# Optimization experiments

Hardware: AMD Instinct MI355X
Metric: run time of the kernel (lower is better)

## Reference

```python
import jax, jax.numpy as jnp
import numpy as np

L_MAX = 6          # L_in = L_out = (0, 6)
N = 2048           # batch / node count
C = 256            # channels (channel_wise => in == out)
NUM_ORDERS = (L_MAX + 1) ** 2  # 49


def _so2_indices(lmax):
    """Replicates equitorch _so2_indices for L_in = L_out = (0, lmax)."""
    entries = []
    widx = 0
    for l_out in range(lmax + 1):
        for l_in in range(lmax + 1):
            for m_w in range(-min(l_out, l_in), min(l_out, l_in) + 1):
                pairs = [(-abs(m_w), -m_w), (abs(m_w), m_w)] if m_w != 0 else [(0, 0)]
                for m_out, m_in in pairs:
                    i_out = l_out * l_out + l_out + m_out  # degree_order_to_index, l_min=0
                    i_in = l_in * l_in + l_in + m_in
                    sign = -1.0 if (m_out > 0 and m_in < 0) else 1.0
                    entries.append((i_out, i_in, l_in, l_out, sign, widx))
                widx += 1
    entries.sort()
    M_out = np.array([e[0] for e in entries], np.int32)
    M_in = np.array([e[1] for e in entries], np.int32)
    sign = np.array([e[4] for e in entries], np.float32)
    w_idx = np.array([e[5] for e in entries], np.int32)
    return M_out, M_in, sign, w_idx, widx


def setup_inputs() -> dict:
    key = jax.random.key(0)
    k1, k2 = jax.random.split(key)
    M_out, M_in, sign, w_idx, num_weights = _so2_indices(L_MAX)
    x = jax.random.normal(k1, (N, NUM_ORDERS, C), dtype=jnp.float32)
    weight = jax.random.normal(k2, (1, num_weights, C), dtype=jnp.float32)
    return {
        "x": x,
        "weight": weight,
        "weight_sign": jnp.asarray(sign),
        "M_in": jnp.asarray(M_in),
        "M_out": jnp.asarray(M_out),
        "weight_index": jnp.asarray(w_idx),
    }


def reference(x, weight, weight_sign, M_in, M_out, weight_index):
    # gather input orders: [N, P, C], P = 413 gathered (m_out, m_in) pairs
    X = x[:, M_in, :]
    # gather per-(l_out,l_in,m) channel-wise weights and apply sign: [1, P, C]
    W = weight[:, weight_index, :] * weight_sign[None, :, None]
    out = X * W  # channel-wise product
    # scatter-add into output orders: [N, num_orders_out, C]
    return jnp.zeros((x.shape[0], NUM_ORDERS, x.shape[2]), x.dtype).at[:, M_out, :].add(out)
```

## Files before the change

### kernel.cpp

```cpp
#include <hip/hip_runtime.h>


#define LMAX 6
#define NORD 49
#define NENT 413
#define C4   64
#define NW   8
#define BLK  512

struct Meta {
  unsigned packed[NENT];
  int gstart[NORD + 1];
  int wbeg[NW + 1];
};

constexpr Meta make_meta() {
  Meta m{};
  int io[NENT] = {}, ii[NENT] = {}, wi[NENT] = {}, sg[NENT] = {};
  int cnt = 0, widx = 0;
  for (int lo = 0; lo <= LMAX; ++lo) {
    for (int li = 0; li <= LMAX; ++li) {
      int mn = lo < li ? lo : li;
      for (int mw = -mn; mw <= mn; ++mw) {
        if (mw == 0) {
          io[cnt] = lo * lo + lo; ii[cnt] = li * li + li;
          wi[cnt] = widx; sg[cnt] = 0; ++cnt;
        } else {
          int a = mw > 0 ? mw : -mw;
          io[cnt] = lo * lo + lo - a; ii[cnt] = li * li + li - mw;
          wi[cnt] = widx; sg[cnt] = 0; ++cnt;
          io[cnt] = lo * lo + lo + a; ii[cnt] = li * li + li + mw;
          wi[cnt] = widx; sg[cnt] = (mw < 0) ? 1 : 0; ++cnt;
        }
        ++widx;
      }
    }
  }
  int slot[NORD * NORD];
  for (int k = 0; k < NORD * NORD; ++k) slot[k] = -1;
  for (int e = 0; e < cnt; ++e) slot[io[e] * NORD + ii[e]] = e;
  int order[NENT] = {};
  int s = 0;
  for (int k = 0; k < NORD * NORD; ++k)
    if (slot[k] >= 0) order[s++] = slot[k];
  int gc[NORD] = {};
  for (int e = 0; e < cnt; ++e) gc[io[e]]++;
  m.gstart[0] = 0;
  for (int g = 0; g < NORD; ++g) m.gstart[g + 1] = m.gstart[g] + gc[g];
  for (int t = 0; t < cnt; ++t) {
    int e = order[t];
    m.packed[t] = (unsigned)ii[e] | ((unsigned)wi[e] << 8) | ((unsigned)sg[e] << 31);
  }
  m.wbeg[0] = 0; m.wbeg[NW] = NORD;
  for (int y = 1; y < NW; ++y) {
    int target = (cnt * y) / NW;
    int g = m.wbeg[y - 1] + 1;
    while (g < NORD && m.gstart[g] < target) ++g;
    if (g - 1 > m.wbeg[y - 1] &&
        (m.gstart[g] - target) > (target - m.gstart[g - 1])) --g;
    int maxg = NORD - (NW - y);
    if (g > maxg) g = maxg;
    m.wbeg[y] = g;
  }
  return m;
}

static constexpr Meta g_meta = make_meta();

template <int E, int E1>
struct Ent {
  __device__ static inline void run(float4& acc, const float4* __restrict__ xs,
                                    const float4* __restrict__ wg, int lane) {
    constexpr unsigned p = g_meta.packed[E];
    constexpr int mi = (int)(p & 255u);
    constexpr int wix = (int)((p >> 8) & 0x3FFu);
    constexpr bool neg = (p & 0x80000000u) != 0u;
    float4 xv = xs[mi * C4 + lane];
    float4 wv = wg[wix * C4 + lane];
    if constexpr (neg) {
      acc.x = fmaf(-xv.x, wv.x, acc.x);
      acc.y = fmaf(-xv.y, wv.y, acc.y);
      acc.z = fmaf(-xv.z, wv.z, acc.z);
      acc.w = fmaf(-xv.w, wv.w, acc.w);
    } else {
      acc.x = fmaf(xv.x, wv.x, acc.x);
      acc.y = fmaf(xv.y, wv.y, acc.y);
      acc.z = fmaf(xv.z, wv.z, acc.z);
      acc.w = fmaf(xv.w, wv.w, acc.w);
    }
    Ent<E + 1, E1>::run(acc, xs, wg, lane);
  }
};
template <int E1>
struct Ent<E1, E1> {
  __device__ static inline void run(float4&, const float4*, const float4*, int) {}
};

template <int G, int G1>
struct Grp {
  __device__ static inline void run(const float4* __restrict__ xs,
                                    const float4* __restrict__ wg,
                                    float4* __restrict__ og, int lane) {
    float4 acc = make_float4(0.f, 0.f, 0.f, 0.f);
    Ent<g_meta.gstart[G], g_meta.gstart[G + 1]>::run(acc, xs, wg, lane);
    og[G * C4 + lane] = acc;
    Grp<G + 1, G1>::run(xs, wg, og, lane);
  }
};
template <int G1>
struct Grp<G1, G1> {
  __device__ static inline void run(const float4*, const float4*, float4*, int) {}
};

__global__ __launch_bounds__(BLK, 4) void so2_kernel(
    const float* __restrict__ x, const float* __restrict__ w,
    float* __restrict__ out) {
  __shared__ float4 xs[NORD * C4];
  const int tid = threadIdx.x;
  const int n = blockIdx.x;
  const int wv = tid >> 6;
  const int lane = tid & 63;

  const float4* __restrict__ xg =
      reinterpret_cast<const float4*>(x) + (size_t)n * (NORD * C4);
#pragma unroll
  for (int i = 0; i < 7; ++i) {
    const int slot = i * BLK + wv * 64;
    if (slot < NORD * C4) {
      __builtin_amdgcn_global_load_lds(
          (const __attribute__((address_space(1))) void*)(xg + slot + lane),
          (__attribute__((address_space(3))) void*)(&xs[slot]), 16, 0, 0);
    }
  }
  __syncthreads();

  const float4* __restrict__ wg = reinterpret_cast<const float4*>(w);
  float4* __restrict__ og =
      reinterpret_cast<float4*>(out) + (size_t)n * (NORD * C4);

  switch (wv) {
    case 0: Grp<g_meta.wbeg[0], g_meta.wbeg[1]>::run(xs, wg, og, lane); break;
    case 1: Grp<g_meta.wbeg[1], g_meta.wbeg[2]>::run(xs, wg, og, lane); break;
    case 2: Grp<g_meta.wbeg[2], g_meta.wbeg[3]>::run(xs, wg, og, lane); break;
    case 3: Grp<g_meta.wbeg[3], g_meta.wbeg[4]>::run(xs, wg, og, lane); break;
    case 4: Grp<g_meta.wbeg[4], g_meta.wbeg[5]>::run(xs, wg, og, lane); break;
    case 5: Grp<g_meta.wbeg[5], g_meta.wbeg[6]>::run(xs, wg, og, lane); break;
    case 6: Grp<g_meta.wbeg[6], g_meta.wbeg[7]>::run(xs, wg, og, lane); break;
    case 7: Grp<g_meta.wbeg[7], g_meta.wbeg[8]>::run(xs, wg, og, lane); break;
  }
}

extern "C" void kernel_launch(void* const* d_in, const int* in_sizes, int n_in,
                              void* d_out, int out_size, void* d_ws, size_t ws_size,
                              hipStream_t stream) {
  const float* x = (const float*)d_in[0];
  const float* w = (const float*)d_in[1];
  float* out = (float*)d_out;
  const int n_rows = in_sizes[0] / (NORD * 4 * C4);
  so2_kernel<<<n_rows, BLK, 0, stream>>>(x, w, out);
}
```

Baseline: 215.1 us.

## Drop LDS staging of x and pre-expand signed weights into workspace

Removes the global-to-LDS copy of each node's input rows and the block barrier, so each wave reads x directly from global memory and relies on cache for reuse. When enough workspace is available, a small pre-kernel expands the weights per entry and folds the sign into them, so the main kernel reads a contiguous sign-free weight stream. This adds a second launch and more weight traffic, and repeated x reads now go through L1/L2 instead of LDS. The occupancy hint in the launch bounds is also removed.

```diff
diff --git a/kernel.cpp b/kernel.cpp
--- a/kernel.cpp
+++ b/kernel.cpp
@@ -4,6 +4,7 @@
 #define LMAX 6
 #define NORD 49
 #define NENT 413
+#define NWGT 231
 #define C4   64
 #define NW   8
 #define BLK  512
@@ -66,56 +67,81 @@
 }
 
 static constexpr Meta g_meta = make_meta();
+__constant__ Meta c_meta = make_meta();
 
-template <int E, int E1>
+__global__ __launch_bounds__(256) void so2_expand_w(
+    const float* __restrict__ w, float* __restrict__ wexp) {
+  const int e = blockIdx.x * 4 + (threadIdx.x >> 6);
+  const int lane = threadIdx.x & 63;
+  if (e >= NENT) return;
+  const unsigned p = c_meta.packed[e];
+  const int wix = (int)((p >> 8) & 0x3FFu);
+  const unsigned sbit = p & 0x80000000u;
+  float4 v = reinterpret_cast<const float4*>(w)[wix * C4 + lane];
+  v.x = __uint_as_float(__float_as_uint(v.x) ^ sbit);
+  v.y = __uint_as_float(__float_as_uint(v.y) ^ sbit);
+  v.z = __uint_as_float(__float_as_uint(v.z) ^ sbit);
+  v.w = __uint_as_float(__float_as_uint(v.w) ^ sbit);
+  reinterpret_cast<float4*>(wexp)[e * C4 + lane] = v;
+}
+
+template <bool XW, int E, int E1>
 struct Ent {
-  __device__ static inline void run(float4& acc, const float4* __restrict__ xs,
-                                    const float4* __restrict__ wg, int lane) {
+  __device__ static inline void run(float4& acc, const float4* __restrict__ xg,
+                                    const float4* __restrict__ wp, int lane) {
     constexpr unsigned p = g_meta.packed[E];
     constexpr int mi = (int)(p & 255u);
-    constexpr int wix = (int)((p >> 8) & 0x3FFu);
-    constexpr bool neg = (p & 0x80000000u) != 0u;
-    float4 xv = xs[mi * C4 + lane];
-    float4 wv = wg[wix * C4 + lane];
-    if constexpr (neg) {
-      acc.x = fmaf(-xv.x, wv.x, acc.x);
-      acc.y = fmaf(-xv.y, wv.y, acc.y);
-      acc.z = fmaf(-xv.z, wv.z, acc.z);
-      acc.w = fmaf(-xv.w, wv.w, acc.w);
-    } else {
+    float4 xv = xg[mi * C4 + lane];
+    if constexpr (XW) {
+      float4 wv = wp[E * C4 + lane];
       acc.x = fmaf(xv.x, wv.x, acc.x);
       acc.y = fmaf(xv.y, wv.y, acc.y);
       acc.z = fmaf(xv.z, wv.z, acc.z);
       acc.w = fmaf(xv.w, wv.w, acc.w);
+    } else {
+      constexpr int wix = (int)((p >> 8) & 0x3FFu);
+      constexpr bool neg = (p & 0x80000000u) != 0u;
+      float4 wv = wp[wix * C4 + lane];
+      if constexpr (neg) {
+        acc.x = fmaf(-xv.x, wv.x, acc.x);
+        acc.y = fmaf(-xv.y, wv.y, acc.y);
+        acc.z = fmaf(-xv.z, wv.z, acc.z);
+        acc.w = fmaf(-xv.w, wv.w, acc.w);
+      } else {
+        acc.x = fmaf(xv.x, wv.x, acc.x);
+        acc.y = fmaf(xv.y, wv.y, acc.y);
+        acc.z = fmaf(xv.z, wv.z, acc.z);
+        acc.w = fmaf(xv.w, wv.w, acc.w);
+      }
     }
-    Ent<E + 1, E1>::run(acc, xs, wg, lane);
+    Ent<XW, E + 1, E1>::run(acc, xg, wp, lane);
   }
 };
-template <int E1>
-struct Ent<E1, E1> {
+template <bool XW, int E1>
+struct Ent<XW, E1, E1> {
   __device__ static inline void run(float4&, const float4*, const float4*, int) {}
 };
 
-template <int G, int G1>
+template <bool XW, int G, int G1>
 struct Grp {
-  __device__ static inline void run(const float4* __restrict__ xs,
-                                    const float4* __restrict__ wg,
+  __device__ static inline void run(const float4* __restrict__ xg,
+                                    const float4* __restrict__ wp,
                                     float4* __restrict__ og, int lane) {
     float4 acc = make_float4(0.f, 0.f, 0.f, 0.f);
-    Ent<g_meta.gstart[G], g_meta.gstart[G + 1]>::run(acc, xs, wg, lane);
+    Ent<XW, g_meta.gstart[G], g_meta.gstart[G + 1]>::run(acc, xg, wp, lane);
     og[G * C4 + lane] = acc;
-    Grp<G + 1, G1>::run(xs, wg, og, lane);
+    Grp<XW, G + 1, G1>::run(xg, wp, og, lane);
   }
 };
-template <int G1>
-struct Grp<G1, G1> {
+template <bool XW, int G1>
+struct Grp<XW, G1, G1> {
   __device__ static inline void run(const float4*, const float4*, float4*, int) {}
 };
 
-__global__ __launch_bounds__(BLK, 4) void so2_kernel(
-    const float* __restrict__ x, const float* __restrict__ w,
+template <bool XW>
+__global__ __launch_bounds__(BLK) void so2_kernel(
+    const float* __restrict__ x, const float* __restrict__ wp_,
     float* __restrict__ out) {
-  __shared__ float4 xs[NORD * C4];
   const int tid = threadIdx.x;
   const int n = blockIdx.x;
   const int wv = tid >> 6;
@@ -123,30 +149,19 @@
 
   const float4* __restrict__ xg =
       reinterpret_cast<const float4*>(x) + (size_t)n * (NORD * C4);
-#pragma unroll
-  for (int i = 0; i < 7; ++i) {
-    const int slot = i * BLK + wv * 64;
-    if (slot < NORD * C4) {
-      __builtin_amdgcn_global_load_lds(
-          (const __attribute__((address_space(1))) void*)(xg + slot + lane),
-          (__attribute__((address_space(3))) void*)(&xs[slot]), 16, 0, 0);
-    }
-  }
-  __syncthreads();
-
-  const float4* __restrict__ wg = reinterpret_cast<const float4*>(w);
+  const float4* __restrict__ wp = reinterpret_cast<const float4*>(wp_);
   float4* __restrict__ og =
       reinterpret_cast<float4*>(out) + (size_t)n * (NORD * C4);
 
   switch (wv) {
-    case 0: Grp<g_meta.wbeg[0], g_meta.wbeg[1]>::run(xs, wg, og, lane); break;
-    case 1: Grp<g_meta.wbeg[1], g_meta.wbeg[2]>::run(xs, wg, og, lane); break;
-    case 2: Grp<g_meta.wbeg[2], g_meta.wbeg[3]>::run(xs, wg, og, lane); break;
-    case 3: Grp<g_meta.wbeg[3], g_meta.wbeg[4]>::run(xs, wg, og, lane); break;
-    case 4: Grp<g_meta.wbeg[4], g_meta.wbeg[5]>::run(xs, wg, og, lane); break;
-    case 5: Grp<g_meta.wbeg[5], g_meta.wbeg[6]>::run(xs, wg, og, lane); break;
-    case 6: Grp<g_meta.wbeg[6], g_meta.wbeg[7]>::run(xs, wg, og, lane); break;
-    case 7: Grp<g_meta.wbeg[7], g_meta.wbeg[8]>::run(xs, wg, og, lane); break;
+    case 0: Grp<XW, g_meta.wbeg[0], g_meta.wbeg[1]>::run(xg, wp, og, lane); break;
+    case 1: Grp<XW, g_meta.wbeg[1], g_meta.wbeg[2]>::run(xg, wp, og, lane); break;
+    case 2: Grp<XW, g_meta.wbeg[2], g_meta.wbeg[3]>::run(xg, wp, og, lane); break;
+    case 3: Grp<XW, g_meta.wbeg[3], g_meta.wbeg[4]>::run(xg, wp, og, lane); break;
+    case 4: Grp<XW, g_meta.wbeg[4], g_meta.wbeg[5]>::run(xg, wp, og, lane); break;
+    case 5: Grp<XW, g_meta.wbeg[5], g_meta.wbeg[6]>::run(xg, wp, og, lane); break;
+    case 6: Grp<XW, g_meta.wbeg[6], g_meta.wbeg[7]>::run(xg, wp, og, lane); break;
+    case 7: Grp<XW, g_meta.wbeg[7], g_meta.wbeg[8]>::run(xg, wp, og, lane); break;
   }
 }
 
@@ -157,5 +172,12 @@
   const float* w = (const float*)d_in[1];
   float* out = (float*)d_out;
   const int n_rows = in_sizes[0] / (NORD * 4 * C4);
-  so2_kernel<<<n_rows, BLK, 0, stream>>>(x, w, out);
+  const size_t need = (size_t)NENT * C4 * sizeof(float4);
+  if (ws_size >= need) {
+    float* wexp = (float*)d_ws;
+    so2_expand_w<<<(NENT + 3) / 4, 256, 0, stream>>>(w, wexp);
+    so2_kernel<true><<<n_rows, BLK, 0, stream>>>(x, wexp, out);
+  } else {
+    so2_kernel<false><<<n_rows, BLK, 0, stream>>>(x, w, out);
+  }
 }
```

Measured after the change: 231.4 us. +7.6%, slower.
